# Kernel optimization log

Measured on AMD Instinct MI355X. Metric: run time of the kernel, lower is better.

## Reference

```python
import jax, jax.numpy as jnp
import numpy as np
import math

B, S, D, H, DFF = 4, 1024, 1024, 16, 4096
DK = D // H
EPS = 1e-6


def setup_inputs() -> dict:
    key = jax.random.key(0)
    ks = jax.random.split(key, 8)
    sc = 1.0 / math.sqrt(D)
    return {
        "x": jax.random.normal(ks[0], (B, S, D), jnp.float32),
        "src_mask": jnp.ones((B, 1, 1, S), jnp.int32),
        "wq": jax.random.normal(ks[1], (D, D), jnp.float32) * sc,
        "bq": jnp.zeros((D,), jnp.float32),
        "wk": jax.random.normal(ks[2], (D, D), jnp.float32) * sc,
        "bk": jnp.zeros((D,), jnp.float32),
        "wv": jax.random.normal(ks[3], (D, D), jnp.float32) * sc,
        "bv": jnp.zeros((D,), jnp.float32),
        "wo": jax.random.normal(ks[4], (D, D), jnp.float32) * sc,
        "bo": jnp.zeros((D,), jnp.float32),
        "w1": jax.random.normal(ks[5], (D, DFF), jnp.float32) * sc,
        "b1": jnp.zeros((DFF,), jnp.float32),
        "w2": jax.random.normal(ks[6], (DFF, D), jnp.float32) * (1.0 / math.sqrt(DFF)),
        "b2": jnp.zeros((D,), jnp.float32),
        "alpha1": jnp.ones((1,), jnp.float32),
        "beta1": jnp.zeros((1,), jnp.float32),
        "alpha2": jnp.ones((1,), jnp.float32),
        "beta2": jnp.zeros((1,), jnp.float32),
    }


def layer_norm(x, alpha, beta):
    # Faithful to the custom LayerNormalization: scalar alpha/beta,
    # torch std (unbiased, ddof=1), eps added to std (not variance).
    mean = jnp.mean(x, axis=-1, keepdims=True)
    std = jnp.std(x, axis=-1, keepdims=True, ddof=1)
    return alpha * (x - mean) / (std + EPS) + beta


def encoder_block(x, src_mask, wq, bq, wk, bk, wv, bv, wo, bo,
                  w1, b1, w2, b2, alpha1, beta1, alpha2, beta2):
    # --- residual 1: pre-norm self-attention (dropout = 0 / eval mode) ---
    xn = layer_norm(x, alpha1, beta1)
    q = (xn @ wq + bq).reshape(B, S, H, DK).transpose(0, 2, 1, 3)  # bhsd
    k = (xn @ wk + bk).reshape(B, S, H, DK).transpose(0, 2, 1, 3)
    v = (xn @ wv + bv).reshape(B, S, H, DK).transpose(0, 2, 1, 3)
    scores = jnp.einsum("bhqd,bhkd->bhqk", q, k) / math.sqrt(DK)
    scores = jnp.where(src_mask == 0, jnp.float32(-1e9), scores)
    attn = jax.nn.softmax(scores, axis=-1)
    ctx = jnp.einsum("bhqk,bhkd->bhqd", attn, v)
    ctx = ctx.transpose(0, 2, 1, 3).reshape(B, S, D)
    x = x + (ctx @ wo + bo)
    # --- residual 2: pre-norm feed-forward ---
    xn2 = layer_norm(x, alpha2, beta2)
    ff = jax.nn.relu(xn2 @ w1 + b1) @ w2 + b2
    return x + ff


def reference(x, src_mask, wq, bq, wk, bk, wv, bv, wo, bo,
              w1, b1, w2, b2, alpha1, beta1, alpha2, beta2):
    return encoder_block(x, src_mask, wq, bq, wk, bk, wv, bv, wo, bo,
                         w1, b1, w2, b2, alpha1, beta1, alpha2, beta2)
```

## Files before the change

### kernel.cpp

```cpp
#include <hip/hip_runtime.h>
#include <hip/hip_bf16.h>
#include <stdint.h>


#define Bq 4
#define Sq 1024
#define Dq 1024
#define Hq 16
#define DKq 64
#define DFFq 4096
#define Mq 4096

typedef unsigned short u16;
typedef __attribute__((ext_vector_type(4))) float f32x4;
typedef __attribute__((ext_vector_type(8))) short bf16x8;
typedef __attribute__((ext_vector_type(4))) unsigned short u16x4;

__device__ __forceinline__ u16 f2b(float f) {
  unsigned int u = __builtin_bit_cast(unsigned int, f);
  u += 0x7FFFu + ((u >> 16) & 1u);
  return (u16)(u >> 16);
}

__device__ __forceinline__ void gload_lds16(const void* g, void* l) {
  __builtin_amdgcn_global_load_lds(
      reinterpret_cast<__attribute__((address_space(1))) void*>(
          reinterpret_cast<uintptr_t>(g)),
      reinterpret_cast<__attribute__((address_space(3))) void*>(
          reinterpret_cast<uintptr_t>(l)),
      16, 0, 0);
}

#define MFMA16(a, b, c) __builtin_amdgcn_mfma_f32_16x16x32_bf16((a), (b), (c), 0, 0, 0)

__global__ __launch_bounds__(256) void cast_transpose(
    const float* __restrict__ in, u16* __restrict__ out, int K, int N) {
  __shared__ float tile[32][33];
  const int n0 = blockIdx.x * 32, k0 = blockIdx.y * 32;
  const int tx = threadIdx.x & 31, ty = threadIdx.x >> 5;
#pragma unroll
  for (int i = 0; i < 32; i += 8)
    tile[ty + i][tx] = in[(int64_t)(k0 + ty + i) * N + (n0 + tx)];
  __syncthreads();
#pragma unroll
  for (int i = 0; i < 32; i += 8)
    out[(int64_t)(n0 + ty + i) * K + (k0 + tx)] = f2b(tile[tx][ty + i]);
}

__global__ void pack_bias(const float* __restrict__ bq, const float* __restrict__ bk,
                          const float* __restrict__ bv, float* __restrict__ out) {
  int i = blockIdx.x * 256 + threadIdx.x;
  const float* src = (i < 1024) ? bq : (i < 2048 ? bk : bv);
  out[i] = src[i & 1023];
}

__global__ __launch_bounds__(256) void layernorm_k(
    const float* __restrict__ x, const float* __restrict__ alpha,
    const float* __restrict__ beta, u16* __restrict__ out) {
  const int row = blockIdx.x;
  const float4 v = ((const float4*)(x + (int64_t)row * 1024))[threadIdx.x];
  float s = v.x + v.y + v.z + v.w;
  float sq = v.x * v.x + v.y * v.y + v.z * v.z + v.w * v.w;
#pragma unroll
  for (int off = 1; off < 64; off <<= 1) {
    s += __shfl_xor(s, off, 64);
    sq += __shfl_xor(sq, off, 64);
  }
  __shared__ float ss[4], ssq[4];
  const int wid = threadIdx.x >> 6;
  if ((threadIdx.x & 63) == 0) { ss[wid] = s; ssq[wid] = sq; }
  __syncthreads();
  s = ss[0] + ss[1] + ss[2] + ss[3];
  sq = ssq[0] + ssq[1] + ssq[2] + ssq[3];
  const float mean = s * (1.0f / 1024.0f);
  float var = (sq - 1024.0f * mean * mean) * (1.0f / 1023.0f);
  var = fmaxf(var, 0.0f);
  const float inv = alpha[0] / (sqrtf(var) + 1e-6f);
  const float bt = beta[0];
  u16x4 o;
  o[0] = f2b((v.x - mean) * inv + bt);
  o[1] = f2b((v.y - mean) * inv + bt);
  o[2] = f2b((v.z - mean) * inv + bt);
  o[3] = f2b((v.w - mean) * inv + bt);
  *(u16x4*)(out + (int64_t)row * 1024 + threadIdx.x * 4) = o;
}

template <bool OUT_BF16, bool RELU, bool RES>
__global__ __launch_bounds__(256) void gemm_bt(
    const u16* __restrict__ A, const u16* __restrict__ Bt,
    const float* __restrict__ bias, const float* __restrict__ res,
    void* __restrict__ Cout, int Ndim, int K) {
  __shared__ u16 Alds[128 * 32];
  __shared__ u16 Blds[128 * 32];
  const int tid = threadIdx.x;
  const int wid = tid >> 6, lane = tid & 63;
  const int bm0 = blockIdx.y * 128, bn0 = blockIdx.x * 128;
  const int wm = (wid >> 1) * 64, wn = (wid & 1) * 64;
  const int lrow = lane & 15, lg = lane >> 4;

  f32x4 acc[4][4] = {};

  const int srow = tid >> 2;
  const int skoff = (tid & 3) * 8;
  const u16* Ag = A + (int64_t)(bm0 + srow) * K + skoff;
  const u16* Bg = Bt + (int64_t)(bn0 + srow) * K + skoff;
  char* AldsB0 = (char*)Alds + wid * 64 * 16;
  char* AldsB1 = (char*)Alds + (256 + wid * 64) * 16;
  char* BldsB0 = (char*)Blds + wid * 64 * 16;
  char* BldsB1 = (char*)Blds + (256 + wid * 64) * 16;
  const int64_t half = (int64_t)64 * K;

  const int nK = K >> 5;
  for (int kt = 0; kt < nK; ++kt) {
    __syncthreads();
    gload_lds16(Ag, AldsB0);
    gload_lds16(Ag + half, AldsB1);
    gload_lds16(Bg, BldsB0);
    gload_lds16(Bg + half, BldsB1);
    Ag += 32; Bg += 32;
    __syncthreads();
    bf16x8 af[4], bfr[4];
#pragma unroll
    for (int f = 0; f < 4; ++f) {
      af[f] = *(const bf16x8*)&Alds[(wm + f * 16 + lrow) * 32 + lg * 8];
      bfr[f] = *(const bf16x8*)&Blds[(wn + f * 16 + lrow) * 32 + lg * 8];
    }
#pragma unroll
    for (int mf = 0; mf < 4; ++mf)
#pragma unroll
      for (int nf = 0; nf < 4; ++nf)
        acc[mf][nf] = MFMA16(af[mf], bfr[nf], acc[mf][nf]);
  }

#pragma unroll
  for (int mf = 0; mf < 4; ++mf) {
#pragma unroll
    for (int nf = 0; nf < 4; ++nf) {
      const int col = bn0 + wn + nf * 16 + lrow;
      const float bv = bias[col];
#pragma unroll
      for (int r = 0; r < 4; ++r) {
        const int row = bm0 + wm + mf * 16 + lg * 4 + r;
        float v = acc[mf][nf][r] + bv;
        if (RELU) v = fmaxf(v, 0.0f);
        if (RES) v += res[(int64_t)row * Ndim + col];
        if (OUT_BF16)
          ((u16*)Cout)[(int64_t)row * Ndim + col] = f2b(v);
        else
          ((float*)Cout)[(int64_t)row * Ndim + col] = v;
      }
    }
  }
}

__global__ __launch_bounds__(256) void attention_k(
    const u16* __restrict__ qkv, const int* __restrict__ mask,
    u16* __restrict__ ctxout) {
  const int bh = blockIdx.y;
  const int b = bh >> 4, h = bh & 15;
  const int q0 = blockIdx.x * 64;
  const int tid = threadIdx.x, wid = tid >> 6, lane = tid & 63;
  const int lrow = lane & 15, lg = lane >> 4;

  __shared__ u16 Klds[64 * 64];
  __shared__ u16 Vtlds[64 * 72];
  __shared__ u16 Plds[4][16 * 72];

  const int64_t rs = 3072;
  const u16* Qb = qkv + (int64_t)(b * 1024) * rs + h * 64;
  const u16* Kb = Qb + 1024;
  const u16* Vb = Qb + 2048;

  bf16x8 qf[2];
  {
    const u16* qp = Qb + (int64_t)(q0 + wid * 16 + lrow) * rs + lg * 8;
    qf[0] = *(const bf16x8*)qp;
    qf[1] = *(const bf16x8*)(qp + 32);
  }

  float m[4], l[4];
  f32x4 ctx[4] = {};
#pragma unroll
  for (int r = 0; r < 4; ++r) { m[r] = -1e30f; l[r] = 0.0f; }

  for (int kt = 0; kt < 16; ++kt) {
    const int sk0 = kt * 64;
    __syncthreads();
    {
      const int rr = tid >> 3, dof = (tid & 7) * 8;
      const u16* g = Kb + (int64_t)(sk0 + rr) * rs + dof;
      gload_lds16(g, (char*)Klds + wid * 64 * 16);
      gload_lds16(g + 32 * rs, (char*)Klds + (256 + wid * 64) * 16);
    }
    {
      const int d0 = (tid & 15) * 4;
      const int sl = tid >> 4;
#pragma unroll
      for (int i = 0; i < 4; ++i) {
        const int s = sl + i * 16;
        const u16x4 vv = *(const u16x4*)(Vb + (int64_t)(sk0 + s) * rs + d0);
#pragma unroll
        for (int j = 0; j < 4; ++j) Vtlds[(d0 + j) * 72 + s] = vv[j];
      }
    }
    __syncthreads();

    f32x4 sa[4];
#pragma unroll
    for (int nf = 0; nf < 4; ++nf) {
      f32x4 a = {};
      bf16x8 kf0 = *(const bf16x8*)&Klds[(nf * 16 + lrow) * 64 + lg * 8];
      bf16x8 kf1 = *(const bf16x8*)&Klds[(nf * 16 + lrow) * 64 + 32 + lg * 8];
      a = MFMA16(qf[0], kf0, a);
      a = MFMA16(qf[1], kf1, a);
      sa[nf] = a;
    }
#pragma unroll
    for (int nf = 0; nf < 4; ++nf) {
      const int mval = mask[b * 1024 + sk0 + nf * 16 + lrow];
#pragma unroll
      for (int r = 0; r < 4; ++r) {
        const float sv = sa[nf][r] * 0.125f;
        sa[nf][r] = (mval == 0) ? -1e9f : sv;
      }
    }
    float fac[4];
#pragma unroll
    for (int r = 0; r < 4; ++r) {
      float mx = fmaxf(fmaxf(sa[0][r], sa[1][r]), fmaxf(sa[2][r], sa[3][r]));
#pragma unroll
      for (int off = 1; off < 16; off <<= 1) mx = fmaxf(mx, __shfl_xor(mx, off, 64));
      const float mn = fmaxf(m[r], mx);
      fac[r] = __expf(m[r] - mn);
      m[r] = mn;
    }
    float rsum[4] = {0.f, 0.f, 0.f, 0.f};
    u16 pb[4][4];
#pragma unroll
    for (int nf = 0; nf < 4; ++nf)
#pragma unroll
      for (int r = 0; r < 4; ++r) {
        const float p = __expf(sa[nf][r] - m[r]);
        rsum[r] += p;
        pb[nf][r] = f2b(p);
      }
#pragma unroll
    for (int r = 0; r < 4; ++r) {
      float t = rsum[r];
#pragma unroll
      for (int off = 1; off < 16; off <<= 1) t += __shfl_xor(t, off, 64);
      l[r] = l[r] * fac[r] + t;
#pragma unroll
      for (int df = 0; df < 4; ++df) ctx[df][r] *= fac[r];
    }
    u16* P = &Plds[wid][0];
#pragma unroll
    for (int nf = 0; nf < 4; ++nf)
#pragma unroll
      for (int r = 0; r < 4; ++r)
        P[(lg * 4 + r) * 72 + nf * 16 + lrow] = pb[nf][r];
    __syncthreads();
    bf16x8 pf0 = *(const bf16x8*)&P[lrow * 72 + lg * 8];
    bf16x8 pf1 = *(const bf16x8*)&P[lrow * 72 + 32 + lg * 8];
#pragma unroll
    for (int df = 0; df < 4; ++df) {
      bf16x8 vf0 = *(const bf16x8*)&Vtlds[(df * 16 + lrow) * 72 + lg * 8];
      bf16x8 vf1 = *(const bf16x8*)&Vtlds[(df * 16 + lrow) * 72 + 32 + lg * 8];
      ctx[df] = MFMA16(pf0, vf0, ctx[df]);
      ctx[df] = MFMA16(pf1, vf1, ctx[df]);
    }
  }
#pragma unroll
  for (int df = 0; df < 4; ++df)
#pragma unroll
    for (int r = 0; r < 4; ++r) {
      const int row = b * 1024 + q0 + wid * 16 + lg * 4 + r;
      const int col = h * 64 + df * 16 + lrow;
      ctxout[(int64_t)row * 1024 + col] = f2b(ctx[df][r] / l[r]);
    }
}

extern "C" void kernel_launch(void* const* d_in, const int* in_sizes, int n_in,
                              void* d_out, int out_size, void* d_ws, size_t ws_size,
                              hipStream_t stream) {
  (void)in_sizes; (void)n_in; (void)out_size; (void)ws_size;
  const float* x      = (const float*)d_in[0];
  const int*   mask   = (const int*)d_in[1];
  const float* wq     = (const float*)d_in[2];
  const float* bq     = (const float*)d_in[3];
  const float* wk     = (const float*)d_in[4];
  const float* bk     = (const float*)d_in[5];
  const float* wv     = (const float*)d_in[6];
  const float* bv     = (const float*)d_in[7];
  const float* wo     = (const float*)d_in[8];
  const float* bo     = (const float*)d_in[9];
  const float* w1     = (const float*)d_in[10];
  const float* b1     = (const float*)d_in[11];
  const float* w2     = (const float*)d_in[12];
  const float* b2     = (const float*)d_in[13];
  const float* alpha1 = (const float*)d_in[14];
  const float* beta1  = (const float*)d_in[15];
  const float* alpha2 = (const float*)d_in[16];
  const float* beta2  = (const float*)d_in[17];
  float* out = (float*)d_out;

  char* ws = (char*)d_ws;
  u16*   wqkvT = (u16*)ws;                 ws += (size_t)3072 * 1024 * 2;
  u16*   woT   = (u16*)ws;                 ws += (size_t)1024 * 1024 * 2;
  u16*   w1T   = (u16*)ws;                 ws += (size_t)4096 * 1024 * 2;
  u16*   w2T   = (u16*)ws;                 ws += (size_t)1024 * 4096 * 2;
  float* bqkv  = (float*)ws;               ws += 16384;
  u16*   xn    = (u16*)ws;                 ws += (size_t)4096 * 1024 * 2;
  u16*   qkv   = (u16*)ws;                 ws += (size_t)4096 * 3072 * 2;
  u16*   ctx   = (u16*)ws;                 ws += (size_t)4096 * 1024 * 2;
  float* x2    = (float*)ws;               ws += (size_t)4096 * 1024 * 4;
  u16*   hbuf  = qkv;

  const dim3 blk(256);
  cast_transpose<<<dim3(32, 32), blk, 0, stream>>>(wq, wqkvT, 1024, 1024);
  cast_transpose<<<dim3(32, 32), blk, 0, stream>>>(wk, wqkvT + 1024 * 1024, 1024, 1024);
  cast_transpose<<<dim3(32, 32), blk, 0, stream>>>(wv, wqkvT + 2048 * 1024, 1024, 1024);
  cast_transpose<<<dim3(32, 32), blk, 0, stream>>>(wo, woT, 1024, 1024);
  cast_transpose<<<dim3(128, 32), blk, 0, stream>>>(w1, w1T, 1024, 4096);
  cast_transpose<<<dim3(32, 128), blk, 0, stream>>>(w2, w2T, 4096, 1024);
  pack_bias<<<dim3(12), blk, 0, stream>>>(bq, bk, bv, bqkv);
  layernorm_k<<<4096, blk, 0, stream>>>(x, alpha1, beta1, xn);
  gemm_bt<true, false, false><<<dim3(24, 32), blk, 0, stream>>>(
      xn, wqkvT, bqkv, nullptr, qkv, 3072, 1024);
  attention_k<<<dim3(16, 64), blk, 0, stream>>>(qkv, mask, ctx);
  gemm_bt<false, false, true><<<dim3(8, 32), blk, 0, stream>>>(
      ctx, woT, bo, x, x2, 1024, 1024);
  layernorm_k<<<4096, blk, 0, stream>>>(x2, alpha2, beta2, xn);
  gemm_bt<true, true, false><<<dim3(32, 32), blk, 0, stream>>>(
      xn, w1T, b1, nullptr, hbuf, 4096, 1024);
  gemm_bt<false, false, true><<<dim3(8, 32), blk, 0, stream>>>(
      hbuf, w2T, b2, x2, out, 1024, 4096);
}
```

Before: 463.1 us.

## Pre-transpose V, swizzle attention LDS tiles, and use narrower GEMM tiles for N=1024

Adds a separate kernel that transposes V per head into a contiguous [bh][d][s] buffer. Attention can then load K and V tiles with direct global-to-LDS copies using an XOR swizzle in place of scalar scatter stores, and it drops one barrier around the P tile. The GEMM becomes templated on tile width, and the two N=1024 projections use 64-wide tiles to double the block count for better CU occupancy. This costs an extra kernel launch and an extra round trip of V through memory, and the removed barrier relies on each wave writing and reading only its own P region.

```diff
diff --git a/kernel.cpp b/kernel.cpp
--- a/kernel.cpp
+++ b/kernel.cpp
@@ -2,14 +2,6 @@
 #include <hip/hip_bf16.h>
 #include <stdint.h>
 
-
-#define Bq 4
-#define Sq 1024
-#define Dq 1024
-#define Hq 16
-#define DKq 64
-#define DFFq 4096
-#define Mq 4096
 
 typedef unsigned short u16;
 typedef __attribute__((ext_vector_type(4))) float f32x4;
@@ -52,6 +44,24 @@
   int i = blockIdx.x * 256 + threadIdx.x;
   const float* src = (i < 1024) ? bq : (i < 2048 ? bk : bv);
   out[i] = src[i & 1023];
+}
+
+__global__ __launch_bounds__(256) void transpose_v(
+    const u16* __restrict__ qkv, u16* __restrict__ vt) {
+  __shared__ u16 t[32][33];
+  const int bh = blockIdx.z;
+  const int b = bh >> 4, h = bh & 15;
+  const int s0 = blockIdx.x * 32, d0 = blockIdx.y * 32;
+  const int tx = threadIdx.x & 31, ty = threadIdx.x >> 5;
+  const u16* src = qkv + (int64_t)(b * 1024) * 3072 + 2048 + h * 64;
+#pragma unroll
+  for (int i = 0; i < 32; i += 8)
+    t[ty + i][tx] = src[(int64_t)(s0 + ty + i) * 3072 + d0 + tx];
+  __syncthreads();
+  u16* dst = vt + (int64_t)bh * 64 * 1024;
+#pragma unroll
+  for (int i = 0; i < 32; i += 8)
+    dst[(int64_t)(d0 + ty + i) * 1024 + s0 + tx] = t[tx][ty + i];
 }
 
 __global__ __launch_bounds__(256) void layernorm_k(
@@ -85,20 +95,21 @@
   *(u16x4*)(out + (int64_t)row * 1024 + threadIdx.x * 4) = o;
 }
 
-template <bool OUT_BF16, bool RELU, bool RES>
+template <int BN, bool OUT_BF16, bool RELU, bool RES>
 __global__ __launch_bounds__(256) void gemm_bt(
     const u16* __restrict__ A, const u16* __restrict__ Bt,
     const float* __restrict__ bias, const float* __restrict__ res,
     void* __restrict__ Cout, int Ndim, int K) {
+  constexpr int NF = BN / 32;
   __shared__ u16 Alds[128 * 32];
-  __shared__ u16 Blds[128 * 32];
+  __shared__ u16 Blds[BN * 32];
   const int tid = threadIdx.x;
   const int wid = tid >> 6, lane = tid & 63;
-  const int bm0 = blockIdx.y * 128, bn0 = blockIdx.x * 128;
-  const int wm = (wid >> 1) * 64, wn = (wid & 1) * 64;
+  const int bm0 = blockIdx.y * 128, bn0 = blockIdx.x * BN;
+  const int wm = (wid >> 1) * 64, wn = (wid & 1) * (BN / 2);
   const int lrow = lane & 15, lg = lane >> 4;
 
-  f32x4 acc[4][4] = {};
+  f32x4 acc[4][NF] = {};
 
   const int srow = tid >> 2;
   const int skoff = (tid & 3) * 8;
@@ -116,26 +127,27 @@
     gload_lds16(Ag, AldsB0);
     gload_lds16(Ag + half, AldsB1);
     gload_lds16(Bg, BldsB0);
-    gload_lds16(Bg + half, BldsB1);
+    if (BN == 128) gload_lds16(Bg + half, BldsB1);
     Ag += 32; Bg += 32;
     __syncthreads();
-    bf16x8 af[4], bfr[4];
-#pragma unroll
-    for (int f = 0; f < 4; ++f) {
+    bf16x8 af[4], bfr[NF];
+#pragma unroll
+    for (int f = 0; f < 4; ++f)
       af[f] = *(const bf16x8*)&Alds[(wm + f * 16 + lrow) * 32 + lg * 8];
+#pragma unroll
+    for (int f = 0; f < NF; ++f)
       bfr[f] = *(const bf16x8*)&Blds[(wn + f * 16 + lrow) * 32 + lg * 8];
-    }
 #pragma unroll
     for (int mf = 0; mf < 4; ++mf)
 #pragma unroll
-      for (int nf = 0; nf < 4; ++nf)
+      for (int nf = 0; nf < NF; ++nf)
         acc[mf][nf] = MFMA16(af[mf], bfr[nf], acc[mf][nf]);
   }
 
 #pragma unroll
   for (int mf = 0; mf < 4; ++mf) {
 #pragma unroll
-    for (int nf = 0; nf < 4; ++nf) {
+    for (int nf = 0; nf < NF; ++nf) {
       const int col = bn0 + wn + nf * 16 + lrow;
       const float bv = bias[col];
 #pragma unroll
@@ -154,8 +166,8 @@
 }
 
 __global__ __launch_bounds__(256) void attention_k(
-    const u16* __restrict__ qkv, const int* __restrict__ mask,
-    u16* __restrict__ ctxout) {
+    const u16* __restrict__ qkv, const u16* __restrict__ vt,
+    const int* __restrict__ mask, u16* __restrict__ ctxout) {
   const int bh = blockIdx.y;
   const int b = bh >> 4, h = bh & 15;
   const int q0 = blockIdx.x * 64;
@@ -163,13 +175,13 @@
   const int lrow = lane & 15, lg = lane >> 4;
 
   __shared__ u16 Klds[64 * 64];
-  __shared__ u16 Vtlds[64 * 72];
-  __shared__ u16 Plds[4][16 * 72];
+  __shared__ u16 Vtlds[64 * 64];
+  __shared__ u16 Plds[4][16 * 68];
 
   const int64_t rs = 3072;
   const u16* Qb = qkv + (int64_t)(b * 1024) * rs + h * 64;
   const u16* Kb = Qb + 1024;
-  const u16* Vb = Qb + 2048;
+  const u16* Vtb = vt + (int64_t)bh * 64 * 1024;
 
   bf16x8 qf[2];
   {
@@ -178,6 +190,18 @@
     qf[1] = *(const bf16x8*)(qp + 32);
   }
 
+  const int c0 = wid * 64 + lane, c1 = 256 + c0;
+  const int r0 = c0 >> 3, r1 = c1 >> 3;
+  const int gq0 = (c0 & 7) ^ (r0 & 7), gq1 = (c1 & 7) ^ (r1 & 7);
+  char* KldsB0 = (char*)Klds + wid * 64 * 16;
+  char* KldsB1 = (char*)Klds + (256 + wid * 64) * 16;
+  char* VldsB0 = (char*)Vtlds + wid * 64 * 16;
+  char* VldsB1 = (char*)Vtlds + (256 + wid * 64) * 16;
+  const u16* Kg0 = Kb + (int64_t)r0 * rs + gq0 * 8;
+  const u16* Kg1 = Kb + (int64_t)r1 * rs + gq1 * 8;
+  const u16* Vg0 = Vtb + r0 * 1024 + gq0 * 8;
+  const u16* Vg1 = Vtb + r1 * 1024 + gq1 * 8;
+
   float m[4], l[4];
   f32x4 ctx[4] = {};
 #pragma unroll
@@ -186,31 +210,20 @@
   for (int kt = 0; kt < 16; ++kt) {
     const int sk0 = kt * 64;
     __syncthreads();
-    {
-      const int rr = tid >> 3, dof = (tid & 7) * 8;
-      const u16* g = Kb + (int64_t)(sk0 + rr) * rs + dof;
-      gload_lds16(g, (char*)Klds + wid * 64 * 16);
-      gload_lds16(g + 32 * rs, (char*)Klds + (256 + wid * 64) * 16);
-    }
-    {
-      const int d0 = (tid & 15) * 4;
-      const int sl = tid >> 4;
-#pragma unroll
-      for (int i = 0; i < 4; ++i) {
-        const int s = sl + i * 16;
-        const u16x4 vv = *(const u16x4*)(Vb + (int64_t)(sk0 + s) * rs + d0);
-#pragma unroll
-        for (int j = 0; j < 4; ++j) Vtlds[(d0 + j) * 72 + s] = vv[j];
-      }
-    }
+    gload_lds16(Kg0 + (int64_t)sk0 * rs, KldsB0);
+    gload_lds16(Kg1 + (int64_t)sk0 * rs, KldsB1);
+    gload_lds16(Vg0 + sk0, VldsB0);
+    gload_lds16(Vg1 + sk0, VldsB1);
     __syncthreads();
 
     f32x4 sa[4];
 #pragma unroll
     for (int nf = 0; nf < 4; ++nf) {
+      const int srow = nf * 16 + lrow;
+      const char* kr = (const char*)Klds + srow * 128;
+      bf16x8 kf0 = *(const bf16x8*)(kr + ((lg ^ (srow & 7)) * 16));
+      bf16x8 kf1 = *(const bf16x8*)(kr + (((4 | lg) ^ (srow & 7)) * 16));
       f32x4 a = {};
-      bf16x8 kf0 = *(const bf16x8*)&Klds[(nf * 16 + lrow) * 64 + lg * 8];
-      bf16x8 kf1 = *(const bf16x8*)&Klds[(nf * 16 + lrow) * 64 + 32 + lg * 8];
       a = MFMA16(qf[0], kf0, a);
       a = MFMA16(qf[1], kf1, a);
       sa[nf] = a;
@@ -258,14 +271,15 @@
     for (int nf = 0; nf < 4; ++nf)
 #pragma unroll
       for (int r = 0; r < 4; ++r)
-        P[(lg * 4 + r) * 72 + nf * 16 + lrow] = pb[nf][r];
-    __syncthreads();
-    bf16x8 pf0 = *(const bf16x8*)&P[lrow * 72 + lg * 8];
-    bf16x8 pf1 = *(const bf16x8*)&P[lrow * 72 + 32 + lg * 8];
+        P[(lg * 4 + r) * 68 + nf * 16 + lrow] = pb[nf][r];
+    bf16x8 pf0 = *(const bf16x8*)&P[lrow * 68 + lg * 8];
+    bf16x8 pf1 = *(const bf16x8*)&P[lrow * 68 + 32 + lg * 8];
 #pragma unroll
     for (int df = 0; df < 4; ++df) {
-      bf16x8 vf0 = *(const bf16x8*)&Vtlds[(df * 16 + lrow) * 72 + lg * 8];
-      bf16x8 vf1 = *(const bf16x8*)&Vtlds[(df * 16 + lrow) * 72 + 32 + lg * 8];
+      const int drow = df * 16 + lrow;
+      const char* vr = (const char*)Vtlds + drow * 128;
+      bf16x8 vf0 = *(const bf16x8*)(vr + ((lg ^ (drow & 7)) * 16));
+      bf16x8 vf1 = *(const bf16x8*)(vr + (((4 | lg) ^ (drow & 7)) * 16));
       ctx[df] = MFMA16(pf0, vf0, ctx[df]);
       ctx[df] = MFMA16(pf1, vf1, ctx[df]);
     }
@@ -314,6 +328,7 @@
   u16*   qkv   = (u16*)ws;                 ws += (size_t)4096 * 3072 * 2;
   u16*   ctx   = (u16*)ws;                 ws += (size_t)4096 * 1024 * 2;
   float* x2    = (float*)ws;               ws += (size_t)4096 * 1024 * 4;
+  u16*   vtb   = (u16*)ws;                 ws += (size_t)64 * 64 * 1024 * 2;
   u16*   hbuf  = qkv;
 
   const dim3 blk(256);
@@ -325,14 +340,15 @@
   cast_transpose<<<dim3(32, 128), blk, 0, stream>>>(w2, w2T, 4096, 1024);
   pack_bias<<<dim3(12), blk, 0, stream>>>(bq, bk, bv, bqkv);
   layernorm_k<<<4096, blk, 0, stream>>>(x, alpha1, beta1, xn);
-  gemm_bt<true, false, false><<<dim3(24, 32), blk, 0, stream>>>(
+  gemm_bt<128, true, false, false><<<dim3(24, 32), blk, 0, stream>>>(
       xn, wqkvT, bqkv, nullptr, qkv, 3072, 1024);
-  attention_k<<<dim3(16, 64), blk, 0, stream>>>(qkv, mask, ctx);
-  gemm_bt<false, false, true><<<dim3(8, 32), blk, 0, stream>>>(
+  transpose_v<<<dim3(32, 2, 64), blk, 0, stream>>>(qkv, vtb);
+  attention_k<<<dim3(16, 64), blk, 0, stream>>>(qkv, vtb, mask, ctx);
+  gemm_bt<64, false, false, true><<<dim3(16, 32), blk, 0, stream>>>(
       ctx, woT, bo, x, x2, 1024, 1024);
   layernorm_k<<<4096, blk, 0, stream>>>(x2, alpha2, beta2, xn);
-  gemm_bt<true, true, false><<<dim3(32, 32), blk, 0, stream>>>(
+  gemm_bt<128, true, true, false><<<dim3(32, 32), blk, 0, stream>>>(
       xn, w1T, b1, nullptr, hbuf, 4096, 1024);
-  gemm_bt<false, false, true><<<dim3(8, 32), blk, 0, stream>>>(
+  gemm_bt<64, false, false, true><<<dim3(16, 32), blk, 0, stream>>>(
       hbuf, w2T, b2, x2, out, 1024, 4096);
 }
```

Measured after the change: 415.5 us. -10.3%, faster.
